# Kernel tuning notes

Hardware: AMD Instinct MI355X
Metric: run time of the kernel (lower is better)

Reference implementation:

```python
import jax, jax.numpy as jnp
import numpy as np

N_NODES = 100000
N_EDGES = 1600000
IN_CH = 128
HID = 64
HEADS = 4
N_GRAPHS = 64
NEG_SLOPE = 0.2
LN_EPS = 1e-5


def setup_inputs() -> dict:
    key = jax.random.key(0)
    ks = jax.random.split(key, 24)
    C1 = HID // HEADS  # 16 per-head channels for conv1
    inp = {
        "x": jax.random.normal(ks[0], (N_NODES, IN_CH), dtype=jnp.float32),
        "edge_index": jax.random.randint(ks[1], (2, N_EDGES), 0, N_NODES, dtype=jnp.int64),
        "batch": jnp.sort(jax.random.randint(ks[2], (N_NODES,), 0, N_GRAPHS, dtype=jnp.int64)),
        "num_graphs": N_GRAPHS,
        # conv1: GATConv(IN_CH -> C1, heads=HEADS, concat)
        "W1": jax.random.normal(ks[3], (IN_CH, HEADS * C1), dtype=jnp.float32) * 0.05,
        "att_src1": jax.random.normal(ks[4], (HEADS, C1), dtype=jnp.float32) * 0.1,
        "att_dst1": jax.random.normal(ks[5], (HEADS, C1), dtype=jnp.float32) * 0.1,
        "b1": jnp.zeros((HEADS * C1,), dtype=jnp.float32),
        # conv2: GATConv(HID -> HID, heads=1)
        "W2": jax.random.normal(ks[6], (HID, HID), dtype=jnp.float32) * 0.1,
        "att_src2": jax.random.normal(ks[7], (1, HID), dtype=jnp.float32) * 0.1,
        "att_dst2": jax.random.normal(ks[8], (1, HID), dtype=jnp.float32) * 0.1,
        "b2": jnp.zeros((HID,), dtype=jnp.float32),
        "ln_g": jnp.ones((HID,), dtype=jnp.float32),
        "ln_b": jnp.zeros((HID,), dtype=jnp.float32),
        "w_pool": jax.random.normal(ks[9], (HID, 1), dtype=jnp.float32) * 0.1,
        "b_pool": jnp.zeros((1,), dtype=jnp.float32),
        "w_fc1": jax.random.normal(ks[10], (HID, HID), dtype=jnp.float32) * 0.1,
        "b_fc1": jnp.zeros((HID,), dtype=jnp.float32),
        "w_fc2": jax.random.normal(ks[11], (HID, 1), dtype=jnp.float32) * 0.1,
        "b_fc2": jnp.zeros((1,), dtype=jnp.float32),
    }
    return inp


def gat_conv(x, src, dst, n_nodes, W, att_src, att_dst, bias, heads, out_ch):
    """PyG GATConv (add_self_loops already folded into src/dst)."""
    h = (x @ W).reshape(n_nodes, heads, out_ch)         # [N,H,C]
    a_s = jnp.sum(h * att_src[None], axis=-1)           # [N,H]
    a_d = jnp.sum(h * att_dst[None], axis=-1)           # [N,H]
    alpha = jax.nn.leaky_relu(a_s[src] + a_d[dst], NEG_SLOPE)  # [E,H]
    amax = jax.ops.segment_max(alpha, dst, num_segments=n_nodes)
    amax = jnp.where(jnp.isfinite(amax), amax, 0.0)
    ex = jnp.exp(alpha - amax[dst])
    denom = jax.ops.segment_sum(ex, dst, num_segments=n_nodes)
    w = ex / (denom[dst] + 1e-16)                       # segment softmax over in-edges
    msg = h[src] * w[:, :, None]                        # [E,H,C]
    out = jax.ops.segment_sum(msg, dst, num_segments=n_nodes)
    return out.reshape(n_nodes, heads * out_ch) + bias


def reference(x, edge_index, batch, num_graphs, W1, att_src1, att_dst1, b1,
              W2, att_src2, att_dst2, b2, ln_g, ln_b, w_pool, b_pool,
              w_fc1, b_fc1, w_fc2, b_fc2):
    n = x.shape[0]
    loop = jnp.arange(n, dtype=edge_index.dtype)
    src = jnp.concatenate([edge_index[0], loop])
    dst = jnp.concatenate([edge_index[1], loop])

    h = gat_conv(x, src, dst, n, W1, att_src1, att_dst1, b1, HEADS, HID // HEADS)
    h = jax.nn.elu(h)                                   # dropout is identity in eval
    h_res = h
    h = gat_conv(h, src, dst, n, W2, att_src2, att_dst2, b2, 1, HID)
    h = h + h_res
    mu = jnp.mean(h, axis=-1, keepdims=True)
    var = jnp.mean(jnp.square(h - mu), axis=-1, keepdims=True)
    h = (h - mu) / jnp.sqrt(var + LN_EPS) * ln_g + ln_b
    h = jax.nn.elu(h)

    attn = jax.nn.softmax(h @ w_pool + b_pool, axis=0)  # softmax over ALL nodes (dim=0)
    pooled = jax.ops.segment_sum(h * attn, batch, num_segments=num_graphs)  # [G,HID]
    z = jax.nn.elu(pooled @ w_fc1 + b_fc1)
    return z @ w_fc2 + b_fc2                            # [G,1]
```

## Files before the change

kernel.cpp:

```cpp
#include <hip/hip_runtime.h>
#include <math.h>

#define NN 100000
#define NE 1600000
#define ICH 128
#define HID 64
#define NGR 64
#define NB_SCAN 391

__device__ __forceinline__ float lrelu(float x){ return x > 0.f ? x : 0.2f*x; }
__device__ __forceinline__ float eluf(float x){ return x > 0.f ? x : expm1f(x); }

__device__ __forceinline__ float bf2f(unsigned short u){
  return __uint_as_float(((unsigned int)u) << 16);
}
__device__ __forceinline__ unsigned short f2bf(float f){
  unsigned int u = __float_as_uint(f);
  return (unsigned short)((u + 0x7FFF + ((u >> 16) & 1)) >> 16);
}

__device__ __forceinline__ float wsum64(float v){
  #pragma unroll
  for (int m = 32; m >= 1; m >>= 1) v += __shfl_xor(v, m);
  return v;
}
__device__ __forceinline__ float wsum16(float v){
  v += __shfl_xor(v, 8); v += __shfl_xor(v, 4);
  v += __shfl_xor(v, 2); v += __shfl_xor(v, 1);
  return v;
}
__device__ __forceinline__ int wscan_incl(int v){
  const int lane = threadIdx.x & 63;
  #pragma unroll
  for (int d = 1; d < 64; d <<= 1){
    int t = __shfl_up(v, d);
    if (lane >= d) v += t;
  }
  return v;
}

__global__ __launch_bounds__(256) void k_deg(const int* __restrict__ ei_dst,
                                             int* __restrict__ deg)
{
  const int lo = (blockIdx.x & 3) * 25000, hi = lo + 25000;
  const int nb = gridDim.x >> 2, ib = blockIdx.x >> 2;
  for (int e = ib * 256 + threadIdx.x; e < NE; e += nb * 256){
    int d = ei_dst[e];
    if (d >= lo && d < hi) atomicAdd(&deg[d], 1);
  }
}

__global__ __launch_bounds__(256) void k_scanA(const int* __restrict__ deg,
    int* __restrict__ rowptr, int* __restrict__ bsum)
{
  int i = blockIdx.x * 256 + threadIdx.x;
  int v = (i < NN) ? deg[i] : 0;
  int incl = wscan_incl(v);
  __shared__ int wsums[4];
  int w = threadIdx.x >> 6, lane = threadIdx.x & 63;
  if (lane == 63) wsums[w] = incl;
  __syncthreads();
  int off = 0;
  for (int k = 0; k < w; ++k) off += wsums[k];
  if (i < NN) rowptr[i] = incl - v + off;
  if (threadIdx.x == 255) bsum[blockIdx.x] = off + incl;
}

__global__ __launch_bounds__(512) void k_scanB(const int* __restrict__ bsum,
                                               int* __restrict__ boff)
{
  int i = threadIdx.x;
  int v = (i < NB_SCAN) ? bsum[i] : 0;
  int incl = wscan_incl(v);
  __shared__ int wsums[8];
  int w = threadIdx.x >> 6, lane = threadIdx.x & 63;
  if (lane == 63) wsums[w] = incl;
  __syncthreads();
  int off = 0;
  for (int k = 0; k < w; ++k) off += wsums[k];
  if (i < NB_SCAN) boff[i] = incl - v + off;
}

__global__ __launch_bounds__(256) void k_scanC(int* __restrict__ rowptr,
    const int* __restrict__ boff, int* __restrict__ cursor)
{
  int i = blockIdx.x * 256 + threadIdx.x;
  if (i < NN){
    int val = rowptr[i] + boff[blockIdx.x];
    rowptr[i] = val;
    cursor[i] = val;
  }
  if (i == 0) rowptr[NN] = NE;
}

__global__ __launch_bounds__(256) void k_scatter(const int* __restrict__ ei,
    int* __restrict__ cursor, int* __restrict__ csr_src)
{
  const int lo = (blockIdx.x & 7) * 12500, hi = lo + 12500;
  const int nb = gridDim.x >> 3, ib = blockIdx.x >> 3;
  for (int e = ib * 256 + threadIdx.x; e < NE; e += nb * 256){
    int d = ei[NE + e];
    if (d >= lo && d < hi){
      int pos = atomicAdd(&cursor[d], 1);
      csr_src[pos] = ei[e];
    }
  }
}

__global__ __launch_bounds__(256) void k_gemm1(const float* __restrict__ x,
    const float* __restrict__ W1, const float* __restrict__ asw,
    const float* __restrict__ adw, unsigned short* __restrict__ h1b,
    float* __restrict__ as1, float* __restrict__ ad1)
{
  __shared__ float xs[16 * ICH];
  const int t = threadIdx.x;
  const int n0 = blockIdx.x * 16;
  const float4* xg4 = (const float4*)(x + (size_t)n0 * ICH);
  float4* xs4 = (float4*)xs;
  xs4[t]       = xg4[t];
  xs4[t + 256] = xg4[t + 256];
  __syncthreads();

  const int lane = t & 63;
  const float* xr = xs + (t >> 6) * 4 * ICH;
  float a0 = 0.f, a1 = 0.f, a2 = 0.f, a3 = 0.f;
  #pragma unroll 8
  for (int k = 0; k < ICH; ++k){
    const float w = W1[k * HID + lane];
    a0 = fmaf(xr[k],          w, a0);
    a1 = fmaf(xr[ICH + k],    w, a1);
    a2 = fmaf(xr[2*ICH + k],  w, a2);
    a3 = fmaf(xr[3*ICH + k],  w, a3);
  }
  const float sw = asw[lane], dw = adw[lane];
  const int nw = n0 + (t >> 6) * 4;
  float acc[4] = {a0, a1, a2, a3};
  #pragma unroll
  for (int i = 0; i < 4; ++i){
    const int n = nw + i;
    h1b[(size_t)n * HID + lane] = f2bf(acc[i]);
    float ps = wsum16(acc[i] * sw);
    float pd = wsum16(acc[i] * dw);
    if ((lane & 15) == 0){
      as1[n * 4 + (lane >> 4)] = ps;
      ad1[n * 4 + (lane >> 4)] = pd;
    }
  }
}

__global__ __launch_bounds__(256) void k_conv1(const int* __restrict__ rowptr,
    const int* __restrict__ csr_src, const float* __restrict__ as1,
    const float* __restrict__ ad1, const unsigned short* __restrict__ h1b,
    const float* __restrict__ b1, float* __restrict__ hb)
{
  __shared__ float2 buf[256];
  const int t = threadIdx.x;
  const int lane = t & 63;
  const int h = lane >> 4;
  const int m = lane & 15;
  const int woff = t & 192;
  const int n = (blockIdx.x * 256 + t) >> 6;
  const int row0 = __builtin_amdgcn_readfirstlane(rowptr[n]);
  const int row1 = __builtin_amdgcn_readfirstlane(rowptr[n + 1]);
  const float adh = ad1[4 * n + h];
  const float eself = __expf(lrelu(as1[4 * n + h] + adh));
  float acc = eself * bf2f(h1b[((unsigned)n << 6) | lane]);
  float den_p = 0.f;
  const int rbase = woff + (lane & 48);
  for (int base = row0; base < row1; base += 16){
    const int cnt = min(16, row1 - base);
    int s = 0; float e = 0.f;
    if (m < cnt){
      s = csr_src[base + m];
      e = __expf(lrelu(as1[4 * s + h] + adh));
    }
    den_p += e;
    buf[woff + lane] = make_float2(e, __int_as_float(s));
    for (int j = 0; j < cnt; ++j){
      float2 es = buf[rbase + j];
      int sj = __float_as_int(es.y);
      acc = fmaf(bf2f(h1b[((unsigned)sj << 6) | lane]), es.x, acc);
    }
  }
  float den = wsum16(den_p) + eself;
  float o = acc / (den + 1e-16f) + b1[lane];
  hb[((size_t)n << 6) | lane] = eluf(o);
}

__global__ __launch_bounds__(256) void k_gemm2(const float* __restrict__ h,
    const float* __restrict__ W2, const float* __restrict__ asw,
    const float* __restrict__ adw, unsigned short* __restrict__ h2b,
    float* __restrict__ as2, float* __restrict__ ad2)
{
  __shared__ float hs[16 * HID];
  const int t = threadIdx.x;
  const int n0 = blockIdx.x * 16;
  const float4* hg4 = (const float4*)(h + (size_t)n0 * HID);
  float4* hs4 = (float4*)hs;
  hs4[t] = hg4[t];
  __syncthreads();

  const int lane = t & 63;
  const float* hr = hs + (t >> 6) * 4 * HID;
  float a0 = 0.f, a1 = 0.f, a2 = 0.f, a3 = 0.f;
  #pragma unroll 8
  for (int k = 0; k < HID; ++k){
    const float w = W2[k * HID + lane];
    a0 = fmaf(hr[k],          w, a0);
    a1 = fmaf(hr[HID + k],    w, a1);
    a2 = fmaf(hr[2*HID + k],  w, a2);
    a3 = fmaf(hr[3*HID + k],  w, a3);
  }
  const float sw = asw[lane], dw = adw[lane];
  const int nw = n0 + (t >> 6) * 4;
  float acc[4] = {a0, a1, a2, a3};
  #pragma unroll
  for (int i = 0; i < 4; ++i){
    const int n = nw + i;
    h2b[(size_t)n * HID + lane] = f2bf(acc[i]);
    float ps = wsum64(acc[i] * sw);
    float pd = wsum64(acc[i] * dw);
    if (lane == 0){ as2[n] = ps; ad2[n] = pd; }
  }
}

__global__ __launch_bounds__(256) void k_conv2(const int* __restrict__ rowptr,
    const int* __restrict__ csr_src, const float* __restrict__ as2,
    const float* __restrict__ ad2, const unsigned short* __restrict__ h2b,
    const float* __restrict__ b2, float* __restrict__ hb,
    const float* __restrict__ lng, const float* __restrict__ lnb,
    const float* __restrict__ wpool, const float* __restrict__ bpool,
    float* __restrict__ es)
{
  __shared__ float2 buf[256];
  const int t = threadIdx.x;
  const int lane = t & 63;
  const int woff = t & 192;
  const int n = (blockIdx.x * 256 + t) >> 6;
  const int row0 = __builtin_amdgcn_readfirstlane(rowptr[n]);
  const int row1 = __builtin_amdgcn_readfirstlane(rowptr[n + 1]);
  const float adn = ad2[n];
  const float eself = __expf(lrelu(as2[n] + adn));
  float acc = eself * bf2f(h2b[((unsigned)n << 6) | lane]);
  float den_p = 0.f;
  for (int base = row0; base < row1; base += 64){
    const int cnt = min(64, row1 - base);
    int s = 0; float e = 0.f;
    if (lane < cnt){
      s = csr_src[base + lane];
      e = __expf(lrelu(as2[s] + adn));
    }
    den_p += e;
    buf[woff + lane] = make_float2(e, __int_as_float(s));
    for (int j = 0; j < cnt; ++j){
      float2 esv = buf[woff + j];
      int sj = __float_as_int(esv.y);
      acc = fmaf(bf2f(h2b[((unsigned)sj << 6) | lane]), esv.x, acc);
    }
  }
  float den = wsum64(den_p) + eself;
  const size_t idxn = ((size_t)n << 6) | lane;
  float tv = acc / (den + 1e-16f) + b2[lane] + hb[idxn];
  float mu  = wsum64(tv) * (1.f / 64.f);
  float dv  = tv - mu;
  float var = wsum64(dv * dv) * (1.f / 64.f);
  float hv = dv * (1.f / sqrtf(var + 1e-5f)) * lng[lane] + lnb[lane];
  hv = eluf(hv);
  hb[idxn] = hv;
  float sl = wsum64(hv * wpool[lane]) + bpool[0];
  if (lane == 0) es[n] = __expf(sl);
}

__global__ __launch_bounds__(256) void k_sumes(const float* __restrict__ es,
                                               float* __restrict__ S)
{
  float v = 0.f;
  for (int i = blockIdx.x * 256 + threadIdx.x; i < NN; i += gridDim.x * 256)
    v += es[i];
  v = wsum64(v);
  __shared__ float red[4];
  if ((threadIdx.x & 63) == 0) red[threadIdx.x >> 6] = v;
  __syncthreads();
  if (threadIdx.x == 0) atomicAdd(S, red[0] + red[1] + red[2] + red[3]);
}

__global__ __launch_bounds__(256) void k_pool(const float* __restrict__ hf,
    const float* __restrict__ es, const int* __restrict__ batch,
    const float* __restrict__ S, float* __restrict__ pooled)
{
  const int lane = threadIdx.x & 63;
  const int wseg = blockIdx.x * 4 + (threadIdx.x >> 6);
  const int base = wseg * 64;
  if (base >= NN) return;
  const float invS = 1.f / S[0];
  int end = base + 64; if (end > NN) end = NN;
  float acc = 0.f;
  int gprev = batch[base];
  for (int n = base; n < end; ++n){
    int g = batch[n];
    if (g != gprev){
      atomicAdd(&pooled[gprev * HID + lane], acc);
      acc = 0.f; gprev = g;
    }
    acc = fmaf(hf[(size_t)n * HID + lane], es[n] * invS, acc);
  }
  atomicAdd(&pooled[gprev * HID + lane], acc);
}

__global__ __launch_bounds__(64) void k_head(const float* __restrict__ pooled,
    const float* __restrict__ wfc1, const float* __restrict__ bfc1,
    const float* __restrict__ wfc2, const float* __restrict__ bfc2,
    float* __restrict__ out)
{
  const int g = blockIdx.x, j = threadIdx.x;
  const float* pr = pooled + g * HID;
  float acc = bfc1[j];
  #pragma unroll 4
  for (int k = 0; k < HID; ++k) acc = fmaf(pr[k], wfc1[k * HID + j], acc);
  float z = eluf(acc);
  float r = wsum64(z * wfc2[j]);
  if (j == 0) out[g] = r + bfc2[0];
}

extern "C" void kernel_launch(void* const* d_in, const int* in_sizes, int n_in,
                              void* d_out, int out_size, void* d_ws, size_t ws_size,
                              hipStream_t stream)
{
  const float* x     = (const float*)d_in[0];
  const int*   ei    = (const int*)d_in[1];
  const int*   batch = (const int*)d_in[2];
  const float* W1    = (const float*)d_in[4];
  const float* asw1  = (const float*)d_in[5];
  const float* adw1  = (const float*)d_in[6];
  const float* b1    = (const float*)d_in[7];
  const float* W2    = (const float*)d_in[8];
  const float* asw2  = (const float*)d_in[9];
  const float* adw2  = (const float*)d_in[10];
  const float* b2    = (const float*)d_in[11];
  const float* lng   = (const float*)d_in[12];
  const float* lnb   = (const float*)d_in[13];
  const float* wpool = (const float*)d_in[14];
  const float* bpool = (const float*)d_in[15];
  const float* wfc1  = (const float*)d_in[16];
  const float* bfc1  = (const float*)d_in[17];
  const float* wfc2  = (const float*)d_in[18];
  const float* bfc2  = (const float*)d_in[19];

  float* ws = (float*)d_ws;
  float* hb     = ws;
  float* as1    = ws +  6400000;
  float* ad1    = ws +  6800000;
  float* as2    = ws +  7200000;
  float* ad2    = ws +  7300000;
  float* es     = ws +  7400000;
  float* pooled = ws +  7500000;
  float* Ssum   = ws +  7504096;
  unsigned short* hub = (unsigned short*)(ws + 7504100);
  int* iw       = (int*)(ws + 10704100);
  int* rowptr   = iw;
  int* cursor   = iw + 100004;
  int* deg      = iw + 200008;
  int* bsum     = iw + 300008;
  int* boff     = iw + 300520;
  int* csr_src  = iw + 301032;

  hipMemsetAsync(deg, 0, (size_t)NN * 4, stream);
  hipMemsetAsync(pooled, 0, (size_t)NGR * 64 * 4, stream);
  hipMemsetAsync(Ssum, 0, 4, stream);

  k_deg    <<<2048, 256, 0, stream>>>(ei + NE, deg);
  k_scanA  <<<NB_SCAN, 256, 0, stream>>>(deg, rowptr, bsum);
  k_scanB  <<<1, 512, 0, stream>>>(bsum, boff);
  k_scanC  <<<NB_SCAN, 256, 0, stream>>>(rowptr, boff, cursor);
  k_scatter<<<2048, 256, 0, stream>>>(ei, cursor, csr_src);

  k_gemm1<<<6250, 256, 0, stream>>>(x, W1, asw1, adw1, hub, as1, ad1);
  k_conv1<<<25000, 256, 0, stream>>>(rowptr, csr_src, as1, ad1, hub, b1, hb);
  k_gemm2<<<6250, 256, 0, stream>>>(hb, W2, asw2, adw2, hub, as2, ad2);
  k_conv2<<<25000, 256, 0, stream>>>(rowptr, csr_src, as2, ad2, hub, b2, hb,
                                     lng, lnb, wpool, bpool, es);
  k_sumes<<<128, 256, 0, stream>>>(es, Ssum);
  k_pool <<<391, 256, 0, stream>>>(hb, es, batch, Ssum, pooled);
  k_head <<<64, 64, 0, stream>>>(pooled, wfc1, bfc1, wfc2, bfc2, (float*)d_out);
}
```

Baseline: 404.6 us.

## Split GAT aggregation into attention, channel-sliced gather, and epilogue kernels

Each fused conv kernel is split into three stages. The first computes per-edge exp weights and denominators and writes them to a buffer. The second does a gather over a feature table stored as four 16-channel slices of bf16 (32-byte rows), so each pass touches a smaller working set. The third is an epilogue that adds the self-loop term, bias and activation (and LayerNorm and pool score for layer 2). This aims to improve cache locality of the random neighbor gathers, at the cost of extra kernel launches, writing and re-reading the edge-weight and partial-sum buffers, and reading the CSR indices four times per layer.

```diff
diff --git a/kernel.cpp b/kernel.cpp
--- a/kernel.cpp
+++ b/kernel.cpp
@@ -7,6 +7,8 @@
 #define HID 64
 #define NGR 64
 #define NB_SCAN 391
+#define SLCH 16
+#define NSL 4
 
 __device__ __forceinline__ float lrelu(float x){ return x > 0.f ? x : 0.2f*x; }
 __device__ __forceinline__ float eluf(float x){ return x > 0.f ? x : expm1f(x); }
@@ -109,7 +111,7 @@
 
 __global__ __launch_bounds__(256) void k_gemm1(const float* __restrict__ x,
     const float* __restrict__ W1, const float* __restrict__ asw,
-    const float* __restrict__ adw, unsigned short* __restrict__ h1b,
+    const float* __restrict__ adw, unsigned short* __restrict__ hs,
     float* __restrict__ as1, float* __restrict__ ad1)
 {
   __shared__ float xs[16 * ICH];
@@ -134,74 +136,111 @@
   }
   const float sw = asw[lane], dw = adw[lane];
   const int nw = n0 + (t >> 6) * 4;
+  const int sl = lane >> 4, ch = lane & 15;
   float acc[4] = {a0, a1, a2, a3};
   #pragma unroll
   for (int i = 0; i < 4; ++i){
     const int n = nw + i;
-    h1b[(size_t)n * HID + lane] = f2bf(acc[i]);
+    hs[(size_t)sl * (NN * SLCH) + (size_t)n * SLCH + ch] = f2bf(acc[i]);
     float ps = wsum16(acc[i] * sw);
     float pd = wsum16(acc[i] * dw);
-    if ((lane & 15) == 0){
-      as1[n * 4 + (lane >> 4)] = ps;
-      ad1[n * 4 + (lane >> 4)] = pd;
-    }
-  }
-}
-
-__global__ __launch_bounds__(256) void k_conv1(const int* __restrict__ rowptr,
+    if (ch == 0){
+      as1[n * 4 + sl] = ps;
+      ad1[n * 4 + sl] = pd;
+    }
+  }
+}
+
+__global__ __launch_bounds__(256) void k_att1(const int* __restrict__ rowptr,
     const int* __restrict__ csr_src, const float* __restrict__ as1,
-    const float* __restrict__ ad1, const unsigned short* __restrict__ h1b,
-    const float* __restrict__ b1, float* __restrict__ hb)
-{
-  __shared__ float2 buf[256];
-  const int t = threadIdx.x;
-  const int lane = t & 63;
-  const int h = lane >> 4;
-  const int m = lane & 15;
-  const int woff = t & 192;
+    const float* __restrict__ ad1, float* __restrict__ exn,
+    float* __restrict__ den1, float* __restrict__ eself1)
+{
+  const int t = threadIdx.x, lane = t & 63, h = lane >> 4, m = lane & 15;
   const int n = (blockIdx.x * 256 + t) >> 6;
   const int row0 = __builtin_amdgcn_readfirstlane(rowptr[n]);
   const int row1 = __builtin_amdgcn_readfirstlane(rowptr[n + 1]);
   const float adh = ad1[4 * n + h];
-  const float eself = __expf(lrelu(as1[4 * n + h] + adh));
-  float acc = eself * bf2f(h1b[((unsigned)n << 6) | lane]);
   float den_p = 0.f;
-  const int rbase = woff + (lane & 48);
   for (int base = row0; base < row1; base += 16){
-    const int cnt = min(16, row1 - base);
-    int s = 0; float e = 0.f;
-    if (m < cnt){
-      s = csr_src[base + m];
-      e = __expf(lrelu(as1[4 * s + h] + adh));
-    }
-    den_p += e;
-    buf[woff + lane] = make_float2(e, __int_as_float(s));
-    for (int j = 0; j < cnt; ++j){
-      float2 es = buf[rbase + j];
-      int sj = __float_as_int(es.y);
-      acc = fmaf(bf2f(h1b[((unsigned)sj << 6) | lane]), es.x, acc);
-    }
-  }
+    int idx = base + m;
+    if (idx < row1){
+      int s = csr_src[idx];
+      float e = __expf(lrelu(as1[4 * s + h] + adh));
+      exn[(size_t)h * NE + idx] = e;
+      den_p += e;
+    }
+  }
+  float eself = __expf(lrelu(as1[4 * n + h] + adh));
   float den = wsum16(den_p) + eself;
-  float o = acc / (den + 1e-16f) + b1[lane];
+  if (m == 0){
+    den1[4 * n + h] = den;
+    eself1[4 * n + h] = eself;
+  }
+}
+
+__global__ __launch_bounds__(256) void k_convs(const int* __restrict__ rowptr,
+    const int* __restrict__ csr_src, const float* __restrict__ ex,
+    size_t ex_stride, const unsigned short* __restrict__ hs,
+    float* __restrict__ acc)
+{
+  const int t = threadIdx.x;
+  const int b = blockIdx.x;
+  const int s = b / 25000;
+  const int n = (b % 25000) * 4 + (t >> 6);
+  const int lane = t & 63, eg = lane >> 4, ch = lane & 15;
+  const int row0 = __builtin_amdgcn_readfirstlane(rowptr[n]);
+  const int row1 = __builtin_amdgcn_readfirstlane(rowptr[n + 1]);
+  const float* __restrict__ exs = ex + (size_t)s * ex_stride;
+  const unsigned short* __restrict__ hss = hs + (size_t)s * (NN * SLCH);
+  float a0 = 0.f, a1 = 0.f;
+  for (int base = row0; base < row1; base += 8){
+    int i0 = base + eg, i1 = base + 4 + eg;
+    if (i0 < row1){
+      int sr = csr_src[i0];
+      a0 = fmaf(bf2f(hss[sr * SLCH + ch]), exs[i0], a0);
+    }
+    if (i1 < row1){
+      int sr = csr_src[i1];
+      a1 = fmaf(bf2f(hss[sr * SLCH + ch]), exs[i1], a1);
+    }
+  }
+  float a = a0 + a1;
+  a += __shfl_xor(a, 16);
+  a += __shfl_xor(a, 32);
+  if (eg == 0) acc[((size_t)s * NN + n) * SLCH + ch] = a;
+}
+
+__global__ __launch_bounds__(256) void k_epi1(const float* __restrict__ acc,
+    const unsigned short* __restrict__ hs, const float* __restrict__ den1,
+    const float* __restrict__ eself1, const float* __restrict__ b1,
+    float* __restrict__ hb)
+{
+  const int t = threadIdx.x, lane = t & 63, s = lane >> 4, ch = lane & 15;
+  const int n = (blockIdx.x * 256 + t) >> 6;
+  float a = acc[((size_t)s * NN + n) * SLCH + ch];
+  float hself = bf2f(hs[(size_t)s * (NN * SLCH) + (size_t)n * SLCH + ch]);
+  float den = den1[4 * n + s];
+  float esf = eself1[4 * n + s];
+  float o = (a + esf * hself) / (den + 1e-16f) + b1[lane];
   hb[((size_t)n << 6) | lane] = eluf(o);
 }
 
 __global__ __launch_bounds__(256) void k_gemm2(const float* __restrict__ h,
     const float* __restrict__ W2, const float* __restrict__ asw,
-    const float* __restrict__ adw, unsigned short* __restrict__ h2b,
+    const float* __restrict__ adw, unsigned short* __restrict__ hs,
     float* __restrict__ as2, float* __restrict__ ad2)
 {
-  __shared__ float hs[16 * HID];
+  __shared__ float hsm[16 * HID];
   const int t = threadIdx.x;
   const int n0 = blockIdx.x * 16;
   const float4* hg4 = (const float4*)(h + (size_t)n0 * HID);
-  float4* hs4 = (float4*)hs;
+  float4* hs4 = (float4*)hsm;
   hs4[t] = hg4[t];
   __syncthreads();
 
   const int lane = t & 63;
-  const float* hr = hs + (t >> 6) * 4 * HID;
+  const float* hr = hsm + (t >> 6) * 4 * HID;
   float a0 = 0.f, a1 = 0.f, a2 = 0.f, a3 = 0.f;
   #pragma unroll 8
   for (int k = 0; k < HID; ++k){
@@ -213,54 +252,58 @@
   }
   const float sw = asw[lane], dw = adw[lane];
   const int nw = n0 + (t >> 6) * 4;
+  const int sl = lane >> 4, ch = lane & 15;
   float acc[4] = {a0, a1, a2, a3};
   #pragma unroll
   for (int i = 0; i < 4; ++i){
     const int n = nw + i;
-    h2b[(size_t)n * HID + lane] = f2bf(acc[i]);
+    hs[(size_t)sl * (NN * SLCH) + (size_t)n * SLCH + ch] = f2bf(acc[i]);
     float ps = wsum64(acc[i] * sw);
     float pd = wsum64(acc[i] * dw);
     if (lane == 0){ as2[n] = ps; ad2[n] = pd; }
   }
 }
 
-__global__ __launch_bounds__(256) void k_conv2(const int* __restrict__ rowptr,
+__global__ __launch_bounds__(256) void k_att2(const int* __restrict__ rowptr,
     const int* __restrict__ csr_src, const float* __restrict__ as2,
-    const float* __restrict__ ad2, const unsigned short* __restrict__ h2b,
-    const float* __restrict__ b2, float* __restrict__ hb,
-    const float* __restrict__ lng, const float* __restrict__ lnb,
-    const float* __restrict__ wpool, const float* __restrict__ bpool,
-    float* __restrict__ es)
-{
-  __shared__ float2 buf[256];
-  const int t = threadIdx.x;
-  const int lane = t & 63;
-  const int woff = t & 192;
+    const float* __restrict__ ad2, float* __restrict__ ex2,
+    float* __restrict__ den2, float* __restrict__ eself2)
+{
+  const int t = threadIdx.x, lane = t & 63;
   const int n = (blockIdx.x * 256 + t) >> 6;
   const int row0 = __builtin_amdgcn_readfirstlane(rowptr[n]);
   const int row1 = __builtin_amdgcn_readfirstlane(rowptr[n + 1]);
   const float adn = ad2[n];
-  const float eself = __expf(lrelu(as2[n] + adn));
-  float acc = eself * bf2f(h2b[((unsigned)n << 6) | lane]);
   float den_p = 0.f;
   for (int base = row0; base < row1; base += 64){
-    const int cnt = min(64, row1 - base);
-    int s = 0; float e = 0.f;
-    if (lane < cnt){
-      s = csr_src[base + lane];
-      e = __expf(lrelu(as2[s] + adn));
-    }
-    den_p += e;
-    buf[woff + lane] = make_float2(e, __int_as_float(s));
-    for (int j = 0; j < cnt; ++j){
-      float2 esv = buf[woff + j];
-      int sj = __float_as_int(esv.y);
-      acc = fmaf(bf2f(h2b[((unsigned)sj << 6) | lane]), esv.x, acc);
-    }
-  }
+    int idx = base + lane;
+    if (idx < row1){
+      int sr = csr_src[idx];
+      float e = __expf(lrelu(as2[sr] + adn));
+      ex2[idx] = e;
+      den_p += e;
+    }
+  }
+  float eself = __expf(lrelu(as2[n] + adn));
   float den = wsum64(den_p) + eself;
+  if (lane == 0){ den2[n] = den; eself2[n] = eself; }
+}
+
+__global__ __launch_bounds__(256) void k_epi2(const float* __restrict__ acc,
+    const unsigned short* __restrict__ hs, const float* __restrict__ den2,
+    const float* __restrict__ eself2, const float* __restrict__ b2,
+    float* __restrict__ hb, const float* __restrict__ lng,
+    const float* __restrict__ lnb, const float* __restrict__ wpool,
+    const float* __restrict__ bpool, float* __restrict__ es)
+{
+  const int t = threadIdx.x, lane = t & 63, s = lane >> 4, ch = lane & 15;
+  const int n = (blockIdx.x * 256 + t) >> 6;
+  float a = acc[((size_t)s * NN + n) * SLCH + ch];
+  float hself = bf2f(hs[(size_t)s * (NN * SLCH) + (size_t)n * SLCH + ch]);
+  float den = den2[n];
+  float esf = eself2[n];
   const size_t idxn = ((size_t)n << 6) | lane;
-  float tv = acc / (den + 1e-16f) + b2[lane] + hb[idxn];
+  float tv = (a + esf * hself) / (den + 1e-16f) + b2[lane] + hb[idxn];
   float mu  = wsum64(tv) * (1.f / 64.f);
   float dv  = tv - mu;
   float var = wsum64(dv * dv) * (1.f / 64.f);
@@ -348,15 +391,21 @@
 
   float* ws = (float*)d_ws;
   float* hb     = ws;
-  float* as1    = ws +  6400000;
-  float* ad1    = ws +  6800000;
-  float* as2    = ws +  7200000;
-  float* ad2    = ws +  7300000;
-  float* es     = ws +  7400000;
-  float* pooled = ws +  7500000;
-  float* Ssum   = ws +  7504096;
-  unsigned short* hub = (unsigned short*)(ws + 7504100);
-  int* iw       = (int*)(ws + 10704100);
+  float* acc    = ws +  6400000;
+  float* exn    = ws + 12800000;
+  float* as1    = ws + 19200000;
+  float* ad1    = ws + 19600000;
+  float* den1   = ws + 20000000;
+  float* eself1 = ws + 20400000;
+  float* as2    = ws + 20800000;
+  float* ad2    = ws + 20900000;
+  float* den2   = ws + 21000000;
+  float* eself2 = ws + 21100000;
+  float* es     = ws + 21200000;
+  float* pooled = ws + 21300000;
+  float* Ssum   = ws + 21304096;
+  unsigned short* hs = (unsigned short*)(ws + 21304100);
+  int* iw       = (int*)(ws + 24504100);
   int* rowptr   = iw;
   int* cursor   = iw + 100004;
   int* deg      = iw + 200008;
@@ -374,10 +423,14 @@
   k_scanC  <<<NB_SCAN, 256, 0, stream>>>(rowptr, boff, cursor);
   k_scatter<<<2048, 256, 0, stream>>>(ei, cursor, csr_src);
 
-  k_gemm1<<<6250, 256, 0, stream>>>(x, W1, asw1, adw1, hub, as1, ad1);
-  k_conv1<<<25000, 256, 0, stream>>>(rowptr, csr_src, as1, ad1, hub, b1, hb);
-  k_gemm2<<<6250, 256, 0, stream>>>(hb, W2, asw2, adw2, hub, as2, ad2);
-  k_conv2<<<25000, 256, 0, stream>>>(rowptr, csr_src, as2, ad2, hub, b2, hb,
+  k_gemm1<<<6250, 256, 0, stream>>>(x, W1, asw1, adw1, hs, as1, ad1);
+  k_att1 <<<25000, 256, 0, stream>>>(rowptr, csr_src, as1, ad1, exn, den1, eself1);
+  k_convs<<<100000, 256, 0, stream>>>(rowptr, csr_src, exn, (size_t)NE, hs, acc);
+  k_epi1 <<<25000, 256, 0, stream>>>(acc, hs, den1, eself1, b1, hb);
+  k_gemm2<<<6250, 256, 0, stream>>>(hb, W2, asw2, adw2, hs, as2, ad2);
+  k_att2 <<<25000, 256, 0, stream>>>(rowptr, csr_src, as2, ad2, exn, den2, eself2);
+  k_convs<<<100000, 256, 0, stream>>>(rowptr, csr_src, exn, (size_t)0, hs, acc);
+  k_epi2 <<<25000, 256, 0, stream>>>(acc, hs, den2, eself2, b2, hb,
                                      lng, lnb, wpool, bpool, es);
   k_sumes<<<128, 256, 0, stream>>>(es, Ssum);
   k_pool <<<391, 256, 0, stream>>>(hb, es, batch, Ssum, pooled);
```

Result: slower. 706.1 us (+74.5%).
